# Kernel optimization log

Hardware: AMD Instinct MI355X
Metric: run time of the kernel (lower is better)

The kernel has to match this reference:

```python
import jax, jax.numpy as jnp
import numpy as np

B, H, W = 4, 240, 1216
PROP = 6


def conv2d(x, w, b, pad=0, groups=1):
    out = jax.lax.conv_general_dilated(
        x, w, (1, 1), ((pad, pad), (pad, pad)),
        dimension_numbers=('NCHW', 'OIHW', 'NCHW'),
        feature_group_count=groups)
    return out + b[None, :, None, None]


def affinity(g, ww, wb, ow, ob):
    # g: [B,8,H,W] -> offset [B,18,H,W] (y,x pairs per kernel pt), weight [B,9,H,W]
    wgt = jax.nn.sigmoid(conv2d(g, ww, wb, pad=1))
    wgt = wgt / (jnp.sum(wgt, axis=1, keepdims=True) + 1e-8)
    off = conv2d(g, ow, ob, pad=1)                      # [B,16,H,W]
    off = off.reshape(B, 8, 2, H, W)
    zero = jnp.zeros((B, 1, 2, H, W), off.dtype)
    off = jnp.concatenate([off[:, :4], zero, off[:, 4:]], axis=1)  # zero offset at reference (center) point, idx 4
    return off.reshape(B, 18, H, W), wgt


def bilinear_gather(img, py, px):
    # img [B,H,W]; py/px [B,9,H,W]; zero padding outside the image
    y0 = jnp.floor(py); x0 = jnp.floor(px)
    wy = py - y0; wx = px - x0
    y0i = y0.astype(jnp.int32); x0i = x0.astype(jnp.int32)
    flat = img.reshape(B, -1)
    out = jnp.zeros_like(py)
    for dy, dx, wgt in ((0, 0, (1 - wy) * (1 - wx)), (0, 1, (1 - wy) * wx),
                        (1, 0, wy * (1 - wx)), (1, 1, wy * wx)):
        yy = y0i + dy; xx = x0i + dx
        valid = (yy >= 0) & (yy < H) & (xx >= 0) & (xx < W)
        idx = (jnp.clip(yy, 0, H - 1) * W + jnp.clip(xx, 0, W - 1)).reshape(B, -1)
        v = jnp.take_along_axis(flat, idx, axis=1).reshape(B, 9, H, W)
        out = out + wgt * jnp.where(valid, v, 0.0)
    return out


def mdconv(feat, offset, mask, w3, b3):
    # Modulated deformable conv (DCNv2), 3x3, stride 1, pad 1, dil 1,
    # groups = C = 1, weight w3 [1,1,3,3] (ones), bias b3 [1] (zero).
    off = offset.reshape(B, 9, 2, H, W)
    ky = jnp.repeat(jnp.arange(3), 3).astype(feat.dtype)   # kernel row for k = i*3+j
    kx = jnp.tile(jnp.arange(3), 3).astype(feat.dtype)
    gy = jnp.arange(H, dtype=feat.dtype)
    gx = jnp.arange(W, dtype=feat.dtype)
    py = gy[None, None, :, None] - 1.0 + ky[None, :, None, None] + off[:, :, 0]
    px = gx[None, None, None, :] - 1.0 + kx[None, :, None, None] + off[:, :, 1]
    samp = bilinear_gather(feat[:, 0], py, px)             # [B,9,H,W]
    out = jnp.einsum('bkhw,k->bhw', mask * samp, w3.reshape(9)) + b3[0]
    return out[:, None]


def _forward(feat_init, guidance, attn, aff_w_w, aff_w_b, aff_o_w, aff_o_b,
             w3, b3, proj_w, bn_g, bn_b, c0_w, c0_b, cs_w, cs_b,
             c1_w, c1_b, c2_w, c2_b, csq_w, csq_b, cv_w, cv_b):
    feats = []
    feat = feat_init
    for k in range(PROP):  # fixed, small structural loop (distinct params per step)
        g = guidance[:, 8 * k:8 * (k + 1)]
        off, wgt = affinity(g, aff_w_w[k], aff_w_b[k], aff_o_w[k], aff_o_b[k])
        feat = mdconv(feat, off, wgt, w3, b3)
        feats.append(feat)
    y = jnp.concatenate(feats[3:6], axis=1)                # [B,3,H,W]
    # proj: 1x1 conv (no bias) -> BatchNorm (training-mode stats) -> LeakyReLU(0.2)
    sf = conv2d(y, proj_w, jnp.zeros((6,), y.dtype), pad=0)
    mu = jnp.mean(sf, axis=(0, 2, 3), keepdims=True)
    var = jnp.var(sf, axis=(0, 2, 3), keepdims=True)
    sf = (sf - mu) * jax.lax.rsqrt(var + 1e-5)
    sf = sf * bn_g[None, :, None, None] + bn_b[None, :, None, None]
    sf = jnp.where(sf > 0, sf, 0.2 * sf)
    x = jnp.concatenate([attn, sf], axis=1)                # [B,22,H,W]
    # CrossAttn(dim=22)
    a1 = conv2d(x, c0_w, c0_b, pad=0, groups=22)           # depthwise 1x1
    a2 = conv2d(a1, cs_w, cs_b, pad=1, groups=22)          # depthwise 3x3
    a1 = conv2d(a1, c1_w, c1_b)                            # 22 -> 11
    a2 = conv2d(a2, c2_w, c2_b)                            # 22 -> 11
    ac = jnp.concatenate([a1, a2], axis=1)                 # [B,22,H,W]
    agg = jnp.concatenate([jnp.mean(ac, axis=1, keepdims=True),
                           jnp.max(ac, axis=1, keepdims=True)], axis=1)
    sig = jax.nn.sigmoid(conv2d(agg, csq_w, csq_b, pad=1))
    a = a1 * sig[:, 0:1] + a2 * sig[:, 1:2]
    a = conv2d(a, cv_w, cv_b)                              # [B,3,H,W]
    return jnp.sum(y * a, axis=1, keepdims=True)           # [B,1,H,W]


def setup_inputs() -> dict:
    key = jax.random.key(0)
    ks = jax.random.split(key, 16)
    n = lambda k, s, sc=1.0: sc * jax.random.normal(k, s, dtype=jnp.float32)
    return {
        'feat_init': n(ks[0], (B, 1, H, W)),
        'guidance': n(ks[1], (B, 48, H, W)),
        'attn': n(ks[2], (B, 16, H, W)),
        'feat_fix': n(ks[3], (B, 1, H, W)),
        'aff_w_w': n(ks[4], (PROP, 9, 8, 3, 3), 0.1),
        'aff_w_b': jnp.zeros((PROP, 9), jnp.float32),
        'aff_o_w': n(ks[5], (PROP, 16, 8, 3, 3), 0.05),
        'aff_o_b': jnp.zeros((PROP, 16), jnp.float32),
        'w3': jnp.ones((1, 1, 3, 3), jnp.float32),
        'b3': jnp.zeros((1,), jnp.float32),
        'proj_w': n(ks[6], (6, 3, 1, 1), 0.3),
        'bn_g': jnp.ones((6,), jnp.float32),
        'bn_b': jnp.zeros((6,), jnp.float32),
        'c0_w': n(ks[7], (22, 1, 1, 1), 0.3),
        'c0_b': jnp.zeros((22,), jnp.float32),
        'cs_w': n(ks[8], (22, 1, 3, 3), 0.2),
        'cs_b': jnp.zeros((22,), jnp.float32),
        'c1_w': n(ks[9], (11, 22, 1, 1), 0.2),
        'c1_b': jnp.zeros((11,), jnp.float32),
        'c2_w': n(ks[10], (11, 22, 1, 1), 0.2),
        'c2_b': jnp.zeros((11,), jnp.float32),
        'csq_w': n(ks[11], (2, 2, 3, 3), 0.2),
        'csq_b': jnp.zeros((2,), jnp.float32),
        'cv_w': n(ks[12], (3, 11, 1, 1), 0.2),
        'cv_b': jnp.zeros((3,), jnp.float32),
    }


def reference(feat_init, guidance, attn, feat_fix, aff_w_w, aff_w_b, aff_o_w, aff_o_b,
              w3, b3, proj_w, bn_g, bn_b, c0_w, c0_b, cs_w, cs_b,
              c1_w, c1_b, c2_w, c2_b, csq_w, csq_b, cv_w, cv_b):
    # mask_fix = sign(feat_fix) is computed in the original but never used.
    _ = jnp.sign(feat_fix)
    return _forward(feat_init, guidance, attn, aff_w_w, aff_w_b, aff_o_w, aff_o_b,
                    w3, b3, proj_w, bn_g, bn_b, c0_w, c0_b, cs_w, cs_b,
                    c1_w, c1_b, c2_w, c2_b, csq_w, csq_b, cv_w, cv_b)
```

## Files before the change

kernel.cpp:

```cpp
#include <hip/hip_runtime.h>
#include <hip/hip_bf16.h>
#include <math.h>

#define HH 240
#define WW 1216
#define BATCH 4
#define PROP 6
constexpr int HW = HH * WW;
constexpr int NPIX = BATCH * HW;
constexpr int NPART = 1024;

typedef short short8 __attribute__((ext_vector_type(8)));
typedef float floatx4 __attribute__((ext_vector_type(4)));

__device__ __forceinline__ unsigned short f2bf(float f) {
    unsigned int u = __float_as_uint(f);
    unsigned int r = (u + 0x7FFFu + ((u >> 16) & 1u)) >> 16;
    return (unsigned short)r;
}
__device__ __forceinline__ float bf2f(unsigned short h) {
    return __uint_as_float(((unsigned int)h) << 16);
}

constexpr int CT_STRIDE = 27;
constexpr int SMEM_BYTES = 21792 + 4 * 64 * CT_STRIDE * 4;

__global__ __launch_bounds__(256, 3) void prop_kernel(
    const float* __restrict__ featPrev,
    const float* __restrict__ gbase,
    const float* __restrict__ aw,
    const float* __restrict__ ab,
    const float* __restrict__ ow,
    const float* __restrict__ ob,
    const float* __restrict__ w3,
    const float* __restrict__ b3,
    float* __restrict__ featNext)
{
    __shared__ __attribute__((aligned(16))) unsigned char smem[SMEM_BYTES];
    uint32_t* gpk    = (uint32_t*)smem;
    uint32_t* offtab = (uint32_t*)(smem + 21120);
    float*    wst    = (float*)(smem + 21792);
    float*    ctb    = (float*)(smem + 21792);

    const int tid = threadIdx.x;
    const int x0 = blockIdx.x * 64;
    const int y0t = blockIdx.y * 8;
    const int b = blockIdx.z;
    const float* gb = gbase + (size_t)b * (48 * HW);

    for (int idx = tid; idx < 5280; idx += 256) {
        const int c = idx / 660, rem = idx - c * 660;
        const int row = rem / 66, col = rem - row * 66;
        const int gy = y0t + row - 1, gx = x0 + col - 1;
        float v = 0.0f;
        if (((unsigned)gy < (unsigned)HH) & ((unsigned)gx < (unsigned)WW))
            v = gb[c * HW + gy * WW + gx];
        const unsigned short hi = f2bf(v);
        const unsigned short lo = f2bf(v - bf2f(hi));
        gpk[idx] = ((uint32_t)hi << 16) | lo;
    }
    for (int idx = tid; idx < 3072; idx += 256) {
        const int o = idx / 96, k = idx - o * 96;
        float v = 0.0f;
        if (o < 25 && k < 72) {
            const int c = k / 9, t = k - 9 * c;
            v = (o < 9) ? aw[(o * 8 + c) * 9 + t] : ow[((o - 9) * 8 + c) * 9 + t];
        }
        wst[idx] = v;
    }
    if (tid < 96) {
        const int s = tid >> 5, rem = tid & 31, e = rem >> 2, gq = rem & 3;
        const int k = s * 32 + gq * 8 + e;
        uint32_t off = 0;
        if (k < 72) {
            const int c = k / 9, t = k - 9 * c, dy = t / 3, dx = t - 3 * dy;
            off = (uint32_t)(c * 660 + dy * 66 + dx);
        }
        offtab[tid] = off;
    }
    __syncthreads();

    const int lane = tid & 63, wid = tid >> 6;
    const int grp = lane >> 4, l15 = lane & 15;

    short8 Ah0[3], Ah1[3], Al0[3], Al1[3];
    {
        const int kb = grp * 8;
#pragma unroll
        for (int s = 0; s < 3; ++s) {
            const float* wp0 = &wst[l15 * 96 + s * 32 + kb];
            const float* wp1 = &wst[(16 + l15) * 96 + s * 32 + kb];
            short8 h0, l0, h1, l1;
#pragma unroll
            for (int e = 0; e < 8; ++e) {
                const float v0 = wp0[e];
                const unsigned short hb0 = f2bf(v0);
                h0[e] = (short)hb0;
                l0[e] = (short)f2bf(v0 - bf2f(hb0));
                const float v1 = wp1[e];
                const unsigned short hb1 = f2bf(v1);
                h1[e] = (short)hb1;
                l1[e] = (short)f2bf(v1 - bf2f(hb1));
            }
            Ah0[s] = h0; Al0[s] = l0; Ah1[s] = h1; Al1[s] = l1;
        }
    }

    uint32_t cvaddr[3][8];
#pragma unroll
    for (int s = 0; s < 3; ++s)
#pragma unroll
        for (int e = 0; e < 8; ++e)
            cvaddr[s][e] = (offtab[s * 32 + e * 4 + grp] +
                            (uint32_t)(wid * 132 + l15)) * 4u;

    float abv[9], w3v[9], obv[16];
#pragma unroll
    for (int t = 0; t < 9; ++t) { abv[t] = ab[t]; w3v[t] = w3[t]; }
#pragma unroll
    for (int o = 0; o < 16; ++o) obv[o] = ob[o];
    const float b3v = b3[0];

    __syncthreads();

    float* ct = ctb + wid * (64 * CT_STRIDE);
    const float* fb = featPrev + (size_t)b * HW;
    const int ybase = y0t + wid * 2;
    const unsigned char* gpkB = (const unsigned char*)gpk;

#pragma unroll 1
    for (int r = 0; r < 2; ++r) {
        const int y = ybase + r;
#pragma unroll
        for (int ch = 0; ch < 4; ++ch) {
            floatx4 acc0 = {0.f, 0.f, 0.f, 0.f};
            floatx4 acc1 = {0.f, 0.f, 0.f, 0.f};
#pragma unroll
            for (int s = 0; s < 3; ++s) {
                uint32_t ev[8];
#pragma unroll
                for (int e = 0; e < 8; ++e)
                    ev[e] = *(const uint32_t*)(gpkB + cvaddr[s][e] +
                                               (r * 66 + ch * 16) * 4);
                union { uint32_t u[4]; short8 v; } bh, bl;
#pragma unroll
                for (int i = 0; i < 4; ++i) {
                    bh.u[i] = (ev[2 * i] >> 16) | (ev[2 * i + 1] & 0xFFFF0000u);
                    bl.u[i] = (ev[2 * i] & 0xFFFFu) | (ev[2 * i + 1] << 16);
                }
                acc0 = __builtin_amdgcn_mfma_f32_16x16x32_bf16(Ah0[s], bh.v, acc0, 0, 0, 0);
                acc1 = __builtin_amdgcn_mfma_f32_16x16x32_bf16(Ah1[s], bh.v, acc1, 0, 0, 0);
                acc0 = __builtin_amdgcn_mfma_f32_16x16x32_bf16(Ah0[s], bl.v, acc0, 0, 0, 0);
                acc1 = __builtin_amdgcn_mfma_f32_16x16x32_bf16(Ah1[s], bl.v, acc1, 0, 0, 0);
                acc0 = __builtin_amdgcn_mfma_f32_16x16x32_bf16(Al0[s], bh.v, acc0, 0, 0, 0);
                acc1 = __builtin_amdgcn_mfma_f32_16x16x32_bf16(Al1[s], bh.v, acc1, 0, 0, 0);
            }
            const int pxb = (ch * 16 + l15) * CT_STRIDE;
#pragma unroll
            for (int i = 0; i < 4; ++i) {
                ct[pxb + grp * 4 + i] = acc0[i];
                if (grp * 4 + i < 9)
                    ct[pxb + 16 + grp * 4 + i] = acc1[i];
            }
        }

        const float* cb = ct + lane * CT_STRIDE;
        float av[25];
#pragma unroll
        for (int o = 0; o < 25; ++o) av[o] = cb[o];

        float wg[9], wsum = 1e-8f;
#pragma unroll
        for (int t = 0; t < 9; ++t) {
            const float s = 1.0f / (1.0f + __expf(-(av[t] + abv[t])));
            wg[t] = s;
            wsum += s;
        }
        const float winv = 1.0f / wsum;
        const int x = x0 + lane;

        float sum = 0.0f;
#pragma unroll
        for (int t = 0; t < 9; ++t) {
            float oy, ox;
            if (t < 4)       { oy = av[9 + 2 * t] + obv[2 * t];
                               ox = av[10 + 2 * t] + obv[2 * t + 1]; }
            else if (t == 4) { oy = 0.0f; ox = 0.0f; }
            else             { oy = av[7 + 2 * t] + obv[2 * t - 2];
                               ox = av[8 + 2 * t] + obv[2 * t - 1]; }

            const float py = (float)(y - 1 + (t / 3)) + oy;
            const float px = (float)(x - 1 + (t % 3)) + ox;
            const float fy = floorf(py), fx = floorf(px);
            const float wy = py - fy, wx = px - fx;
            const int iy = (int)fy, ix = (int)fx;
            const int iy1 = iy + 1, ix1 = ix + 1;

            const int ry0 = min(max(iy, 0), HH - 1) * WW;
            const int ry1 = min(max(iy1, 0), HH - 1) * WW;
            const int cx0 = min(max(ix, 0), WW - 1);
            const int cx1 = min(max(ix1, 0), WW - 1);
            const float v00 = fb[ry0 + cx0], v01 = fb[ry0 + cx1];
            const float v10 = fb[ry1 + cx0], v11 = fb[ry1 + cx1];

            const bool vy0 = (unsigned)iy < (unsigned)HH;
            const bool vy1 = (unsigned)iy1 < (unsigned)HH;
            const bool vx0 = (unsigned)ix < (unsigned)WW;
            const bool vx1 = (unsigned)ix1 < (unsigned)WW;
            const float wy0 = 1.0f - wy, wx0 = 1.0f - wx;

            float s = 0.0f;
            s = fmaf((vy0 & vx0) ? wy0 * wx0 : 0.0f, v00, s);
            s = fmaf((vy0 & vx1) ? wy0 * wx  : 0.0f, v01, s);
            s = fmaf((vy1 & vx0) ? wy  * wx0 : 0.0f, v10, s);
            s = fmaf((vy1 & vx1) ? wy  * wx  : 0.0f, v11, s);

            sum = fmaf(wg[t] * w3v[t], s, sum);
        }
        featNext[(size_t)b * HW + (size_t)y * WW + x] = fmaf(winv, sum, b3v);
    }
}

__global__ __launch_bounds__(256) void stats_part(
    const float* __restrict__ y0s, const float* __restrict__ y1s,
    const float* __restrict__ y2s, float* __restrict__ part)
{
    float a[9] = {0, 0, 0, 0, 0, 0, 0, 0, 0};
    const int stride = gridDim.x * 256;
    for (int i = blockIdx.x * 256 + threadIdx.x; i < NPIX; i += stride) {
        const float v0 = y0s[i], v1 = y1s[i], v2 = y2s[i];
        a[0] += v0; a[1] += v1; a[2] += v2;
        a[3] = fmaf(v0, v0, a[3]); a[4] = fmaf(v0, v1, a[4]);
        a[5] = fmaf(v0, v2, a[5]); a[6] = fmaf(v1, v1, a[6]);
        a[7] = fmaf(v1, v2, a[7]); a[8] = fmaf(v2, v2, a[8]);
    }
    __shared__ float red[4][9];
    const int lane = threadIdx.x & 63, wv = threadIdx.x >> 6;
#pragma unroll
    for (int q = 0; q < 9; ++q) {
        float v = a[q];
        for (int o = 32; o; o >>= 1) v += __shfl_down(v, o, 64);
        if (lane == 0) red[wv][q] = v;
    }
    __syncthreads();
    if (threadIdx.x < 9) {
        const int q = threadIdx.x;
        part[blockIdx.x * 9 + q] = red[0][q] + red[1][q] + red[2][q] + red[3][q];
    }
}

__global__ __launch_bounds__(256) void stats_final(
    const float* __restrict__ part, const float* __restrict__ proj_w,
    const float* __restrict__ bn_g, const float* __restrict__ bn_b,
    float* __restrict__ stats)
{
    float a[9] = {0, 0, 0, 0, 0, 0, 0, 0, 0};
    for (int i = threadIdx.x; i < NPART; i += 256) {
#pragma unroll
        for (int q = 0; q < 9; ++q) a[q] += part[i * 9 + q];
    }
    __shared__ float red[4][9];
    const int lane = threadIdx.x & 63, wv = threadIdx.x >> 6;
#pragma unroll
    for (int q = 0; q < 9; ++q) {
        float v = a[q];
        for (int o = 32; o; o >>= 1) v += __shfl_down(v, o, 64);
        if (lane == 0) red[wv][q] = v;
    }
    __syncthreads();
    if (threadIdx.x == 0) {
        float s[9];
#pragma unroll
        for (int q = 0; q < 9; ++q) s[q] = red[0][q] + red[1][q] + red[2][q] + red[3][q];
        const float invN = 1.0f / (float)NPIX;
        const float m0 = s[0] * invN, m1 = s[1] * invN, m2 = s[2] * invN;
        const float E00 = s[3] * invN, E01 = s[4] * invN, E02 = s[5] * invN;
        const float E11 = s[6] * invN, E12 = s[7] * invN, E22 = s[8] * invN;
#pragma unroll
        for (int c = 0; c < 6; ++c) {
            const float p0 = proj_w[c * 3], p1 = proj_w[c * 3 + 1], p2 = proj_w[c * 3 + 2];
            const float mu = p0 * m0 + p1 * m1 + p2 * m2;
            const float e2 = p0 * p0 * E00 + p1 * p1 * E11 + p2 * p2 * E22 +
                             2.0f * (p0 * p1 * E01 + p0 * p2 * E02 + p1 * p2 * E12);
            const float var = e2 - mu * mu;
            const float sc = bn_g[c] / sqrtf(var + 1e-5f);
            stats[c] = sc;
            stats[6 + c] = bn_b[c] - mu * sc;
        }
    }
}

__global__ __launch_bounds__(256, 4) void head_kernel(
    const float* __restrict__ y0s, const float* __restrict__ y1s,
    const float* __restrict__ y2s, const float* __restrict__ attn,
    const float* __restrict__ stats,
    const float* __restrict__ proj_w,
    const float* __restrict__ c0_w, const float* __restrict__ c0_b,
    const float* __restrict__ cs_w, const float* __restrict__ cs_b,
    const float* __restrict__ c1_w, const float* __restrict__ c1_b,
    const float* __restrict__ c2_w, const float* __restrict__ c2_b,
    const float* __restrict__ csq_w, const float* __restrict__ csq_b,
    const float* __restrict__ cv_w, const float* __restrict__ cv_b,
    float* __restrict__ out)
{
    __shared__ float ap[22][432];
    __shared__ float aggs[2][340];

    const int tid = threadIdx.x;
    const int b = blockIdx.z;
    const int x0 = blockIdx.x * 32;
    const int y0t = blockIdx.y * 8;

    for (int idx = tid; idx < 432; idx += 256) {
        const int eyl = idx / 36, exl = idx - eyl * 36;
        const int gy = y0t + eyl - 2, gx = x0 + exl - 2;
        float v[22];
        if (((unsigned)gy < (unsigned)HH) & ((unsigned)gx < (unsigned)WW)) {
            const size_t p = (size_t)gy * WW + gx;
            const float* abp = attn + (size_t)b * 16 * HW + p;
#pragma unroll
            for (int c = 0; c < 16; ++c)
                v[c] = fmaf(c0_w[c], abp[(size_t)c * HW], c0_b[c]);
            const float ym0 = y0s[(size_t)b * HW + p];
            const float ym1 = y1s[(size_t)b * HW + p];
            const float ym2 = y2s[(size_t)b * HW + p];
#pragma unroll
            for (int j = 0; j < 6; ++j) {
                const float sraw = proj_w[j * 3] * ym0 + proj_w[j * 3 + 1] * ym1 +
                                   proj_w[j * 3 + 2] * ym2;
                float sf = fmaf(stats[j], sraw, stats[6 + j]);
                sf = sf > 0.0f ? sf : 0.2f * sf;
                v[16 + j] = fmaf(c0_w[16 + j], sf, c0_b[16 + j]);
            }
        } else {
#pragma unroll
            for (int c = 0; c < 22; ++c) v[c] = 0.0f;
        }
#pragma unroll
        for (int c = 0; c < 22; ++c) ap[c][idx] = v[c];
    }
    __syncthreads();

    auto compute_px = [&](int ay, int ax, float* a1, float* a2) {
        const int ey = ay + 1, ex = ax + 1;
#pragma unroll
        for (int j = 0; j < 11; ++j) { a1[j] = c1_b[j]; a2[j] = c2_b[j]; }
#pragma unroll
        for (int c = 0; c < 22; ++c) {
            float dw = cs_b[c];
            float ctr = 0.0f;
#pragma unroll
            for (int t = 0; t < 9; ++t) {
                const float av = ap[c][(ey + t / 3 - 1) * 36 + (ex + t % 3 - 1)];
                dw = fmaf(cs_w[c * 9 + t], av, dw);
                if (t == 4) ctr = av;
            }
#pragma unroll
            for (int j = 0; j < 11; ++j) {
                a1[j] = fmaf(c1_w[j * 22 + c], ctr, a1[j]);
                a2[j] = fmaf(c2_w[j * 22 + c], dw, a2[j]);
            }
        }
    };

    if (tid < 84) {
        int ay, ax;
        if (tid < 34)      { ay = 0; ax = tid; }
        else if (tid < 68) { ay = 9; ax = tid - 34; }
        else { const int s = tid - 68; ay = 1 + (s >> 1); ax = (s & 1) ? 33 : 0; }
        const int gy = y0t + ay - 1, gx = x0 + ax - 1;
        float m0 = 0.0f, m1 = 0.0f;
        if (((unsigned)gy < (unsigned)HH) & ((unsigned)gx < (unsigned)WW)) {
            float a1h[11], a2h[11];
            compute_px(ay, ax, a1h, a2h);
            float s = 0.0f, mx = -INFINITY;
#pragma unroll
            for (int j = 0; j < 11; ++j) {
                s += a1h[j] + a2h[j];
                mx = fmaxf(mx, fmaxf(a1h[j], a2h[j]));
            }
            m0 = s * (1.0f / 22.0f);
            m1 = mx;
        }
        aggs[0][ay * 34 + ax] = m0;
        aggs[1][ay * 34 + ax] = m1;
    }

    const int ty = tid >> 5, tx = tid & 31;
    const int ay = ty + 1, ax = tx + 1;
    float a1[11], a2[11];
    compute_px(ay, ax, a1, a2);
    {
        float s = 0.0f, mx = -INFINITY;
#pragma unroll
        for (int j = 0; j < 11; ++j) {
            s += a1[j] + a2[j];
            mx = fmaxf(mx, fmaxf(a1[j], a2[j]));
        }
        aggs[0][ay * 34 + ax] = s * (1.0f / 22.0f);
        aggs[1][ay * 34 + ax] = mx;
    }
    __syncthreads();

    float z0 = csq_b[0], z1 = csq_b[1];
#pragma unroll
    for (int t = 0; t < 9; ++t) {
        const int ai = (ay + t / 3 - 1) * 34 + (ax + t % 3 - 1);
        const float g0 = aggs[0][ai], g1 = aggs[1][ai];
        z0 = fmaf(csq_w[t], g0, fmaf(csq_w[9 + t], g1, z0));
        z1 = fmaf(csq_w[18 + t], g0, fmaf(csq_w[27 + t], g1, z1));
    }
    const float s0 = 1.0f / (1.0f + __expf(-z0));
    const float s1 = 1.0f / (1.0f + __expf(-z1));
    float v0 = cv_b[0], v1 = cv_b[1], v2 = cv_b[2];
#pragma unroll
    for (int j = 0; j < 11; ++j) {
        const float av = a1[j] * s0 + a2[j] * s1;
        v0 = fmaf(cv_w[j], av, v0);
        v1 = fmaf(cv_w[11 + j], av, v1);
        v2 = fmaf(cv_w[22 + j], av, v2);
    }
    const size_t p = (size_t)b * HW + (size_t)(y0t + ty) * WW + (x0 + tx);
    out[p] = y0s[p] * v0 + y1s[p] * v1 + y2s[p] * v2;
}

extern "C" void kernel_launch(void* const* d_in, const int* in_sizes, int n_in,
                              void* d_out, int out_size, void* d_ws, size_t ws_size,
                              hipStream_t stream)
{
    (void)in_sizes; (void)n_in; (void)out_size; (void)ws_size;
    const float* feat_init = (const float*)d_in[0];
    const float* guidance  = (const float*)d_in[1];
    const float* attn      = (const float*)d_in[2];
    const float* aff_w_w   = (const float*)d_in[4];
    const float* aff_w_b   = (const float*)d_in[5];
    const float* aff_o_w   = (const float*)d_in[6];
    const float* aff_o_b   = (const float*)d_in[7];
    const float* w3        = (const float*)d_in[8];
    const float* b3        = (const float*)d_in[9];
    const float* proj_w    = (const float*)d_in[10];
    const float* bn_g      = (const float*)d_in[11];
    const float* bn_b      = (const float*)d_in[12];
    const float* c0_w      = (const float*)d_in[13];
    const float* c0_b      = (const float*)d_in[14];
    const float* cs_w      = (const float*)d_in[15];
    const float* cs_b      = (const float*)d_in[16];
    const float* c1_w      = (const float*)d_in[17];
    const float* c1_b      = (const float*)d_in[18];
    const float* c2_w      = (const float*)d_in[19];
    const float* c2_b      = (const float*)d_in[20];
    const float* csq_w     = (const float*)d_in[21];
    const float* csq_b     = (const float*)d_in[22];
    const float* cv_w      = (const float*)d_in[23];
    const float* cv_b      = (const float*)d_in[24];

    float* ws = (float*)d_ws;
    float* slot[5];
    for (int i = 0; i < 5; ++i) slot[i] = ws + (size_t)i * NPIX;
    float* part  = ws + (size_t)5 * NPIX;
    float* stats = part + (size_t)9 * NPART;

    const dim3 blk(256);
    const dim3 gp(WW / 64, HH / 8, BATCH);

    const int dst_ids[PROP] = {0, 1, 0, 2, 3, 4};
    const float* src = feat_init;
    for (int k = 0; k < PROP; ++k) {
        float* dst = slot[dst_ids[k]];
        prop_kernel<<<gp, blk, 0, stream>>>(
            src, guidance + (size_t)8 * k * HW,
            aff_w_w + (size_t)k * 648, aff_w_b + (size_t)k * 9,
            aff_o_w + (size_t)k * 1152, aff_o_b + (size_t)k * 16,
            w3, b3, dst);
        src = dst;
    }

    stats_part<<<dim3(NPART), blk, 0, stream>>>(slot[2], slot[3], slot[4], part);
    stats_final<<<dim3(1), blk, 0, stream>>>(part, proj_w, bn_g, bn_b, stats);

    head_kernel<<<dim3(WW / 32, HH / 8, BATCH), blk, 0, stream>>>(
        slot[2], slot[3], slot[4], attn, stats, proj_w,
        c0_w, c0_b, cs_w, cs_b, c1_w, c1_b, c2_w, c2_b,
        csq_w, csq_b, cv_w, cv_b, (float*)d_out);
}
```

Before: 642.0 us.

## Vectorize stats and head halo loads with float4 and swizzle head block order

The stats reduction now reads the three inputs as float4, processing four pixels per iteration. The head kernel's halo fill is split into per-channel, per-row float4 load jobs instead of scalar per-pixel loads, which gives wider coalesced reads of attn and the propagation outputs. The head grid is also flattened to 1D with a modulo-8 swizzle of block IDs, likely to spread neighbouring tiles across XCDs. The cost is more index arithmetic and some wasted lanes at the halo edges. Because edge chunks are zeroed when a float4 straddles the border, correctness depends on WW being a multiple of 4 and x0-4 being aligned.

```diff
diff --git a/kernel.cpp b/kernel.cpp
--- a/kernel.cpp
+++ b/kernel.cpp
@@ -226,13 +226,23 @@
     const float* __restrict__ y2s, float* __restrict__ part)
 {
     float a[9] = {0, 0, 0, 0, 0, 0, 0, 0, 0};
+    const int n4 = NPIX / 4;
     const int stride = gridDim.x * 256;
-    for (int i = blockIdx.x * 256 + threadIdx.x; i < NPIX; i += stride) {
-        const float v0 = y0s[i], v1 = y1s[i], v2 = y2s[i];
-        a[0] += v0; a[1] += v1; a[2] += v2;
-        a[3] = fmaf(v0, v0, a[3]); a[4] = fmaf(v0, v1, a[4]);
-        a[5] = fmaf(v0, v2, a[5]); a[6] = fmaf(v1, v1, a[6]);
-        a[7] = fmaf(v1, v2, a[7]); a[8] = fmaf(v2, v2, a[8]);
+    for (int i = blockIdx.x * 256 + threadIdx.x; i < n4; i += stride) {
+        const float4 q0 = ((const float4*)y0s)[i];
+        const float4 q1 = ((const float4*)y1s)[i];
+        const float4 q2 = ((const float4*)y2s)[i];
+        const float v0s[4] = {q0.x, q0.y, q0.z, q0.w};
+        const float v1s[4] = {q1.x, q1.y, q1.z, q1.w};
+        const float v2s[4] = {q2.x, q2.y, q2.z, q2.w};
+#pragma unroll
+        for (int j = 0; j < 4; ++j) {
+            const float v0 = v0s[j], v1 = v1s[j], v2 = v2s[j];
+            a[0] += v0; a[1] += v1; a[2] += v2;
+            a[3] = fmaf(v0, v0, a[3]); a[4] = fmaf(v0, v1, a[4]);
+            a[5] = fmaf(v0, v2, a[5]); a[6] = fmaf(v1, v1, a[6]);
+            a[7] = fmaf(v1, v2, a[7]); a[8] = fmaf(v2, v2, a[8]);
+        }
     }
     __shared__ float red[4][9];
     const int lane = threadIdx.x & 63, wv = threadIdx.x >> 6;
@@ -289,6 +299,11 @@
         }
     }
 }
+
+constexpr int HB_X = WW / 32;
+constexpr int HB_Y = HH / 8;
+constexpr int HB_N = HB_X * HB_Y * BATCH;
+constexpr int HB_CHUNK = HB_N / 8;
 
 __global__ __launch_bounds__(256, 4) void head_kernel(
     const float* __restrict__ y0s, const float* __restrict__ y1s,
@@ -307,37 +322,76 @@
     __shared__ float aggs[2][340];
 
     const int tid = threadIdx.x;
-    const int b = blockIdx.z;
-    const int x0 = blockIdx.x * 32;
-    const int y0t = blockIdx.y * 8;
-
-    for (int idx = tid; idx < 432; idx += 256) {
-        const int eyl = idx / 36, exl = idx - eyl * 36;
-        const int gy = y0t + eyl - 2, gx = x0 + exl - 2;
-        float v[22];
-        if (((unsigned)gy < (unsigned)HH) & ((unsigned)gx < (unsigned)WW)) {
-            const size_t p = (size_t)gy * WW + gx;
-            const float* abp = attn + (size_t)b * 16 * HW + p;
-#pragma unroll
-            for (int c = 0; c < 16; ++c)
-                v[c] = fmaf(c0_w[c], abp[(size_t)c * HW], c0_b[c]);
-            const float ym0 = y0s[(size_t)b * HW + p];
-            const float ym1 = y1s[(size_t)b * HW + p];
-            const float ym2 = y2s[(size_t)b * HW + p];
-#pragma unroll
-            for (int j = 0; j < 6; ++j) {
-                const float sraw = proj_w[j * 3] * ym0 + proj_w[j * 3 + 1] * ym1 +
-                                   proj_w[j * 3 + 2] * ym2;
-                float sf = fmaf(stats[j], sraw, stats[6 + j]);
-                sf = sf > 0.0f ? sf : 0.2f * sf;
-                v[16 + j] = fmaf(c0_w[16 + j], sf, c0_b[16 + j]);
-            }
+    const int bid = blockIdx.x;
+    const int swz = (bid & 7) * HB_CHUNK + (bid >> 3);
+    const int b = swz / (HB_X * HB_Y);
+    const int rem0 = swz - b * (HB_X * HB_Y);
+    const int by = rem0 / HB_X;
+    const int bx = rem0 - by * HB_X;
+    const int x0 = bx * 32;
+    const int y0t = by * 8;
+
+    for (int job = tid; job < 2040; job += 256) {
+        int c = 0, rr, xc;
+        bool isY;
+        if (job < 1920) {
+            c = job / 120;
+            const int rem = job - c * 120;
+            rr = rem / 10; xc = rem - rr * 10;
+            isY = false;
         } else {
-#pragma unroll
-            for (int c = 0; c < 22; ++c) v[c] = 0.0f;
-        }
-#pragma unroll
-        for (int c = 0; c < 22; ++c) ap[c][idx] = v[c];
+            const int rem = job - 1920;
+            rr = rem / 10; xc = rem - rr * 10;
+            isY = true;
+        }
+        const int gy = y0t + rr - 2;
+        const int gxb = x0 - 4 + 4 * xc;
+        const bool gok = ((unsigned)gy < (unsigned)HH) &
+                         ((unsigned)gxb <= (unsigned)(WW - 4));
+        const size_t prow = (size_t)gy * WW + gxb;
+
+        if (!isY) {
+            float4 v4 = {0.f, 0.f, 0.f, 0.f};
+            if (gok)
+                v4 = *(const float4*)&attn[(size_t)b * 16 * HW + (size_t)c * HW + prow];
+            const float w = c0_w[c], bb = c0_b[c];
+            const float vin[4] = {v4.x, v4.y, v4.z, v4.w};
+#pragma unroll
+            for (int j = 0; j < 4; ++j) {
+                const int exl = 4 * xc - 2 + j;
+                if ((unsigned)exl < 36u)
+                    ap[c][rr * 36 + exl] = gok ? fmaf(w, vin[j], bb) : 0.0f;
+            }
+        } else {
+            float4 q0 = {0.f, 0.f, 0.f, 0.f}, q1 = q0, q2 = q0;
+            if (gok) {
+                const size_t p = (size_t)b * HW + prow;
+                q0 = *(const float4*)&y0s[p];
+                q1 = *(const float4*)&y1s[p];
+                q2 = *(const float4*)&y2s[p];
+            }
+            const float v0s[4] = {q0.x, q0.y, q0.z, q0.w};
+            const float v1s[4] = {q1.x, q1.y, q1.z, q1.w};
+            const float v2s[4] = {q2.x, q2.y, q2.z, q2.w};
+#pragma unroll
+            for (int j = 0; j < 4; ++j) {
+                const int exl = 4 * xc - 2 + j;
+                if ((unsigned)exl >= 36u) continue;
+#pragma unroll
+                for (int q = 0; q < 6; ++q) {
+                    float v = 0.0f;
+                    if (gok) {
+                        const float sraw = proj_w[q * 3] * v0s[j] +
+                                           proj_w[q * 3 + 1] * v1s[j] +
+                                           proj_w[q * 3 + 2] * v2s[j];
+                        float sf = fmaf(stats[q], sraw, stats[6 + q]);
+                        sf = sf > 0.0f ? sf : 0.2f * sf;
+                        v = fmaf(c0_w[16 + q], sf, c0_b[16 + q]);
+                    }
+                    ap[16 + q][rr * 36 + exl] = v;
+                }
+            }
+        }
     }
     __syncthreads();
 
@@ -478,7 +532,7 @@
     stats_part<<<dim3(NPART), blk, 0, stream>>>(slot[2], slot[3], slot[4], part);
     stats_final<<<dim3(1), blk, 0, stream>>>(part, proj_w, bn_g, bn_b, stats);
 
-    head_kernel<<<dim3(WW / 32, HH / 8, BATCH), blk, 0, stream>>>(
+    head_kernel<<<dim3(HB_N), blk, 0, stream>>>(
         slot[2], slot[3], slot[4], attn, stats, proj_w,
         c0_w, c0_b, cs_w, cs_b, c1_w, c1_b, c2_w, c2_b,
         csq_w, csq_b, cv_w, cv_b, (float*)d_out);
```

After: 626.3 us. -2.4%, faster.
